# Kernel optimization log

Measured on AMD Instinct MI355X. Metric: run time of the kernel, lower is better.

Reference implementation:

```python
import jax, jax.numpy as jnp
import numpy as np

B, L, D = 8, 8192, 512
TARGET_RATIO = 1.0 / 6.0


def _normalize(v):
    # matches torch F.normalize(dim=-1, eps=1e-12)
    n = jnp.maximum(jnp.linalg.norm(v, axis=-1, keepdims=True), 1e-12)
    return v / n


def _downsample(x, b_hard):
    # vectorized stream compaction, padded to L (static upper bound of L_max)
    Bb, Ll, Dd = x.shape
    cnt = jnp.cumsum(b_hard.astype(jnp.int32), axis=1)
    pos = jnp.where(b_hard > 0.5, cnt - 1, Ll)          # non-selected -> dump slot L
    bidx = jnp.arange(Bb)[:, None]
    out = jnp.zeros((Bb, Ll + 1, Dd), x.dtype).at[bidx, pos].set(x)[:, :Ll]
    counts = cnt[:, -1]
    mask = jnp.arange(Ll)[None, :] < counts[:, None]
    return out, mask


def setup_inputs() -> dict:
    key = jax.random.key(0)
    k1, k2, k3 = jax.random.split(key, 3)
    x = jax.random.normal(k1, (B, L, D), jnp.float32)
    W_q = jax.random.normal(k2, (D, D), jnp.float32) / np.sqrt(D)
    W_k = jax.random.normal(k3, (D, D), jnp.float32) / np.sqrt(D)
    return {"x": x, "W_q": W_q, "W_k": W_k}


def reference(x, W_q, W_k):
    q = _normalize(jnp.einsum('bld,ed->ble', x, W_q))   # nn.Linear: x @ W.T
    k = _normalize(jnp.einsum('bld,ed->ble', x, W_k))
    k_prev = jnp.pad(k[:, :-1, :], ((0, 0), (1, 0), (0, 0)))
    cos_sim = jnp.sum(q * k_prev, axis=-1)               # (B, L)
    p = jnp.clip(0.5 * (1.0 - cos_sim), 0.0, 1.0)
    p = p.at[:, 0].set(1.0)                              # first position always boundary
    b_hard = (p >= 0.5).astype(x.dtype)
    N = 1.0 / TARGET_RATIO
    F_actual = jnp.mean(b_hard)
    G_actual = jnp.mean(p)
    ratio_loss = N / (N - 1.0) * ((N - 1.0) * F_actual * G_actual + (1.0 - F_actual) * (1.0 - G_actual))
    compressed, comp_mask = _downsample(x, b_hard)
    p_compressed, _ = _downsample(p[..., None], b_hard)
    p_compressed = p_compressed[..., 0]
    return (compressed, comp_mask, b_hard, p, p_compressed, ratio_loss)
```

## Files before the change

### kernel.cpp

```cpp
#include <hip/hip_runtime.h>
#include <hip/hip_bf16.h>
#include <math.h>

#define BB 8
#define LL 8192
#define DD 512
#define NROWS (BB * LL)

#define OUT_COMP   0
#define OUT_MASK   33554432
#define OUT_BHARD  33619968
#define OUT_P      33685504
#define OUT_PCOMP  33751040
#define OUT_LOSS   33816576

#define WS_FIXLIST 0
#define WS_FIXCNT  262144
#define WS_COUNTS  262148
#define WS_SUMP    262180
#define WS_SEL     262212
#define WS_SSK     524416
#define WS_SSQ     786560
#define WS_DOT     1048704
#define WS_WQH     1310848
#define WS_WKH     1835136

#define FIX_CAP 65536
#define FIX_TAU 4e-4f

typedef __attribute__((ext_vector_type(8))) _Float16 half8;
typedef __attribute__((ext_vector_type(4))) float f32x4;

static __device__ __forceinline__ void ld_g2l16(const void* g, void* l) {
  __builtin_amdgcn_global_load_lds(
      (const __attribute__((address_space(1))) void*)g,
      (__attribute__((address_space(3))) void*)l, 16, 0, 0);
}

__global__ __launch_bounds__(256) void wsplit(
    const float* __restrict__ Wq, const float* __restrict__ Wk,
    _Float16* __restrict__ wqh, _Float16* __restrict__ wkh,
    float* __restrict__ ssk, float* __restrict__ ssq,
    float* __restrict__ dotb, int* __restrict__ fixcnt) {
  const int t = blockIdx.x * 256 + threadIdx.x;
  if (t == 0) *fixcnt = 0;
  ssk[t] = 0.0f;
  ssq[t] = 0.0f;
  dotb[t] = 0.0f;

  const int m = t >> 15;
  const int c = t & 32767;
  const int kt = c >> 11;
  const int ct = (c >> 6) & 31;
  const int l = c & 63;
  const int n = l & 15;
  const int kblk = l >> 4;
  const int e = ct * 16 + n;
  const int d0 = kt * 32 + kblk * 8;
  const float* src = (m ? Wk : Wq) + (long)e * 512 + d0;
  _Float16* dh = (m ? wkh : wqh) + (long)c * 8;
  float4 v0 = *(const float4*)src;
  float4 v1 = *(const float4*)(src + 4);
  float av[8] = {v0.x, v0.y, v0.z, v0.w, v1.x, v1.y, v1.z, v1.w};
  half8 hi;
#pragma unroll
  for (int j = 0; j < 8; ++j) hi[j] = (_Float16)av[j];
  *(half8*)dh = hi;
}

__global__ __launch_bounds__(256, 2) void gemm_fused(
    const float* __restrict__ x,
    const _Float16* __restrict__ wqh, const _Float16* __restrict__ wkh,
    float* __restrict__ ssqOut, float* __restrict__ sskOut,
    float* __restrict__ dotOut,
    float* __restrict__ qedge, float* __restrict__ kedge) {
  __shared__ _Float16 smem[32768];
  _Float16* AH0 = smem;
  _Float16* AL0 = smem + 4096;
  _Float16* BQ0 = smem + 8192;
  _Float16* BK0 = smem + 12288;
  _Float16* AH1 = smem + 16384;
  _Float16* AL1 = smem + 20480;
  _Float16* BQ1 = smem + 24576;
  _Float16* BK1 = smem + 28672;

  const int tid = threadIdx.x;
  const int lane = tid & 63;
  const int w = tid >> 6;
  const int wrow = w & 1, wcol = w >> 1;
  const int g = lane >> 4, n = lane & 15;
  const int bx0 = blockIdx.x;
  const int bx = ((bx0 & 7) << 8) | (bx0 >> 3);
  const int rb = bx >> 2, cb = bx & 3;
  const long r0 = (long)rb * 128;

  const int arow = ((tid >> 6) << 4) | (tid & 15);
  const int akb = (tid >> 4) & 3;
  const float* ap = x + (r0 + arow) * 512 + akb * 8;

  f32x4 accq[4][4], acck[4][4];
#pragma unroll
  for (int mb = 0; mb < 4; ++mb)
#pragma unroll
    for (int nb = 0; nb < 4; ++nb) {
      accq[mb][nb] = (f32x4){0.f, 0.f, 0.f, 0.f};
      acck[mb][nb] = (f32x4){0.f, 0.f, 0.f, 0.f};
    }

#define STAGE_B(ktv, BQ_, BK_)                                            \
  do {                                                                    \
    const long bb = ((long)((ktv)*32 + cb * 8) << 9) + w * 1024 + lane * 8; \
    ld_g2l16(wqh + bb, (BQ_) + w * 1024);                                 \
    ld_g2l16(wqh + bb + 512, (BQ_) + w * 1024 + 512);                     \
    ld_g2l16(wkh + bb, (BK_) + w * 1024);                                 \
    ld_g2l16(wkh + bb + 512, (BK_) + w * 1024 + 512);                     \
  } while (0)

#define CONV_A(F0, F1, F2, F3, AH_, AL_)                                  \
  do {                                                                    \
    float av0[8] = {F0.x, F0.y, F0.z, F0.w, F1.x, F1.y, F1.z, F1.w};      \
    float av1[8] = {F2.x, F2.y, F2.z, F2.w, F3.x, F3.y, F3.z, F3.w};      \
    half8 h0, h1, l0, l1;                                                 \
    _Pragma("unroll") for (int j = 0; j < 8; ++j) {                       \
      _Float16 a = (_Float16)av0[j];                                      \
      h0[j] = a;                                                          \
      l0[j] = (_Float16)(av0[j] - (float)a);                              \
      _Float16 b = (_Float16)av1[j];                                      \
      h1[j] = b;                                                          \
      l1[j] = (_Float16)(av1[j] - (float)b);                              \
    }                                                                     \
    *(half8*)((AH_) + tid * 8) = h0;                                      \
    *(half8*)((AH_) + (tid + 256) * 8) = h1;                              \
    *(half8*)((AL_) + tid * 8) = l0;                                      \
    *(half8*)((AL_) + (tid + 256) * 8) = l1;                              \
  } while (0)

#define COMPUTE(AH_, AL_, BQ_, BK_)                                       \
  do {                                                                    \
    half8 ah[4], al[4], bq[4], bk[4];                                     \
    _Pragma("unroll") for (int mb = 0; mb < 4; ++mb) {                    \
      const int cm = wrow * 4 + mb;                                       \
      ah[mb] = *(const half8*)((AH_) + (cm * 64 + lane) * 8);             \
      al[mb] = *(const half8*)((AL_) + (cm * 64 + lane) * 8);             \
    }                                                                     \
    _Pragma("unroll") for (int nb = 0; nb < 4; ++nb) {                    \
      bq[nb] = *(const half8*)((BQ_) + ((wcol * 4 + nb) * 64 + lane) * 8);\
      bk[nb] = *(const half8*)((BK_) + ((wcol * 4 + nb) * 64 + lane) * 8);\
    }                                                                     \
    __builtin_amdgcn_s_setprio(1);                                        \
    _Pragma("unroll") for (int nb = 0; nb < 4; ++nb)                      \
        _Pragma("unroll") for (int mb = 0; mb < 4; ++mb) {                \
      accq[mb][nb] = __builtin_amdgcn_mfma_f32_16x16x32_f16(              \
          ah[mb], bq[nb], accq[mb][nb], 0, 0, 0);                         \
      acck[mb][nb] = __builtin_amdgcn_mfma_f32_16x16x32_f16(              \
          ah[mb], bk[nb], acck[mb][nb], 0, 0, 0);                         \
      accq[mb][nb] = __builtin_amdgcn_mfma_f32_16x16x32_f16(              \
          al[mb], bq[nb], accq[mb][nb], 0, 0, 0);                         \
      acck[mb][nb] = __builtin_amdgcn_mfma_f32_16x16x32_f16(              \
          al[mb], bk[nb], acck[mb][nb], 0, 0, 0);                         \
    }                                                                     \
    __builtin_amdgcn_s_setprio(0);                                        \
  } while (0)

  STAGE_B(0, BQ0, BK0);
  float4 pa0 = *(const float4*)(ap);
  float4 pa1 = *(const float4*)(ap + 4);
  float4 pa2 = *(const float4*)(ap + 64 * 512);
  float4 pa3 = *(const float4*)(ap + 64 * 512 + 4);
  CONV_A(pa0, pa1, pa2, pa3, AH0, AL0);
  float4 pb0 = *(const float4*)(ap + 32);
  float4 pb1 = *(const float4*)(ap + 32 + 4);
  float4 pb2 = *(const float4*)(ap + 32 + 64 * 512);
  float4 pb3 = *(const float4*)(ap + 32 + 64 * 512 + 4);
  __syncthreads();

  for (int i = 0; i < 8; ++i) {
    const int kt = 2 * i;
    STAGE_B(kt + 1, BQ1, BK1);
    CONV_A(pb0, pb1, pb2, pb3, AH1, AL1);
    if (i < 7) {
      const float* xp = ap + (kt + 2) * 32;
      pa0 = *(const float4*)(xp);
      pa1 = *(const float4*)(xp + 4);
      pa2 = *(const float4*)(xp + 64 * 512);
      pa3 = *(const float4*)(xp + 64 * 512 + 4);
    }
    COMPUTE(AH0, AL0, BQ0, BK0);
    __syncthreads();
    if (i < 7) {
      STAGE_B(kt + 2, BQ0, BK0);
      CONV_A(pa0, pa1, pa2, pa3, AH0, AL0);
      const float* xp2 = ap + (kt + 3) * 32;
      pb0 = *(const float4*)(xp2);
      pb1 = *(const float4*)(xp2 + 4);
      pb2 = *(const float4*)(xp2 + 64 * 512);
      pb3 = *(const float4*)(xp2 + 64 * 512 + 4);
    }
    COMPUTE(AH1, AL1, BQ1, BK1);
    __syncthreads();
  }

  _Float16* KX = smem;
  const int col0 = wcol * 64 + n;
  const int rbase = wrow * 64;
#pragma unroll
  for (int mb = 0; mb < 4; ++mb)
#pragma unroll
    for (int reg = 0; reg < 4; ++reg) {
      const int rl = rbase + mb * 16 + g * 4 + reg;
#pragma unroll
      for (int nb = 0; nb < 4; ++nb)
        KX[rl * 136 + col0 + nb * 16] = (_Float16)acck[mb][nb][reg];
    }
  __syncthreads();

  if (wrow == 1 && g == 3) {
#pragma unroll
    for (int nb = 0; nb < 4; ++nb)
      kedge[rb * 512 + cb * 128 + col0 + nb * 16] = acck[3][nb][3];
  }
  if (wrow == 0 && g == 0) {
#pragma unroll
    for (int nb = 0; nb < 4; ++nb)
      qedge[rb * 512 + cb * 128 + col0 + nb * 16] = accq[0][nb][0];
  }

#pragma unroll
  for (int mb = 0; mb < 4; ++mb) {
#pragma unroll
    for (int reg = 0; reg < 4; ++reg) {
      const int rl = rbase + mb * 16 + g * 4 + reg;
      const long row = r0 + rl;
      float sq = 0.f, sk = 0.f, dt = 0.f;
#pragma unroll
      for (int nb = 0; nb < 4; ++nb) {
        float qv = accq[mb][nb][reg];
        float kv = acck[mb][nb][reg];
        sq = fmaf(qv, qv, sq);
        sk = fmaf(kv, kv, sk);
        if (rl > 0) {
          float kp = (float)KX[(rl - 1) * 136 + col0 + nb * 16];
          dt = fmaf(qv, kp, dt);
        }
      }
#pragma unroll
      for (int m = 1; m < 16; m <<= 1) {
        sq += __shfl_xor(sq, m, 64);
        sk += __shfl_xor(sk, m, 64);
        dt += __shfl_xor(dt, m, 64);
      }
      if (n == 0) {
        atomicAdd(&ssqOut[row], sq);
        atomicAdd(&sskOut[row], sk);
        if (rl > 0) atomicAdd(&dotOut[row], dt);
      }
    }
  }
#undef STAGE_B
#undef CONV_A
#undef COMPUTE
}

__global__ __launch_bounds__(64) void edgedot(
    const float* __restrict__ qedge, const float* __restrict__ kedge,
    float* __restrict__ dotOut) {
  const int rb = blockIdx.x;
  if (rb == 0) return;
  const long row = (long)rb * 128;
  if ((row & (LL - 1)) == 0) return;
  const int lane = threadIdx.x;
  float dt = 0.f;
#pragma unroll
  for (int c = lane; c < 512; c += 64)
    dt = fmaf(qedge[rb * 512 + c], kedge[(rb - 1) * 512 + c], dt);
#pragma unroll
  for (int m = 1; m < 64; m <<= 1) dt += __shfl_xor(dt, m, 64);
  if (lane == 0) dotOut[row] = dt;
}

__global__ __launch_bounds__(256) void combine(
    const float* __restrict__ ssq, const float* __restrict__ ssk,
    const float* __restrict__ dotb, float* __restrict__ dout,
    int* __restrict__ fixlist, int* __restrict__ fixcnt) {
  const int r = blockIdx.x * 256 + threadIdx.x;
  const int l = r & (LL - 1);
  float p;
  float cosv = 0.0f;
  if (l != 0) {
    float nq = fmaxf(sqrtf(ssq[r]), 1e-12f);
    float nk = fmaxf(sqrtf(ssk[r - 1]), 1e-12f);
    cosv = dotb[r] / (nq * nk);
    p = fminf(fmaxf(0.5f * (1.0f - cosv), 0.0f), 1.0f);
  } else {
    p = 1.0f;
  }
  dout[OUT_P + r] = p;
  dout[OUT_BHARD + r] = (p >= 0.5f) ? 1.0f : 0.0f;
  if (l != 0 && fabsf(cosv) < FIX_TAU) {
    int idx = atomicAdd(fixcnt, 1);
    if (idx < FIX_CAP) fixlist[idx] = r;
  }
}

__global__ __launch_bounds__(256) void fixup(
    const float* __restrict__ x, const float* __restrict__ Wq,
    const float* __restrict__ Wk, float* __restrict__ dout,
    const int* __restrict__ fixlist, const int* __restrict__ fixcnt) {
  __shared__ float xr[512], xp[512];
  __shared__ double red[3][256];
  const int t = threadIdx.x;
  int nfix = *fixcnt;
  if (nfix > FIX_CAP) nfix = FIX_CAP;

  for (int idx = blockIdx.x; idx < nfix; idx += gridDim.x) {
    const int r = fixlist[idx];
    for (int d = t; d < 512; d += 256) {
      xr[d] = x[(long)r * 512 + d];
      xp[d] = x[(long)(r - 1) * 512 + d];
    }
    __syncthreads();
    double ssq = 0.0, ssk = 0.0, dot = 0.0;
    for (int e = t; e < 512; e += 256) {
      const float* wq = Wq + (long)e * 512;
      const float* wk = Wk + (long)e * 512;
      double q = 0.0, k = 0.0;
      for (int d = 0; d < 512; ++d) {
        q = fma((double)xr[d], (double)wq[d], q);
        k = fma((double)xp[d], (double)wk[d], k);
      }
      ssq += q * q;
      ssk += k * k;
      dot += q * k;
    }
    red[0][t] = ssq;
    red[1][t] = ssk;
    red[2][t] = dot;
    __syncthreads();
    for (int s = 128; s > 0; s >>= 1) {
      if (t < s) {
        red[0][t] += red[0][t + s];
        red[1][t] += red[1][t + s];
        red[2][t] += red[2][t + s];
      }
      __syncthreads();
    }
    if (t == 0) {
      double nq = sqrt(red[0][0]);
      double nk = sqrt(red[1][0]);
      if (nq < 1e-12) nq = 1e-12;
      if (nk < 1e-12) nk = 1e-12;
      float c = (float)(red[2][0] / (nq * nk));
      float p = fminf(fmaxf(0.5f * (1.0f - c), 0.0f), 1.0f);
      dout[OUT_P + r] = p;
      dout[OUT_BHARD + r] = (p >= 0.5f) ? 1.0f : 0.0f;
    }
    __syncthreads();
  }
}

__global__ __launch_bounds__(256) void scanb(
    float* __restrict__ dout, int* __restrict__ sel,
    int* __restrict__ counts, float* __restrict__ sump) {
  __shared__ int wtot[4];
  __shared__ float wps[4];
  const int b = blockIdx.x;
  const int t = threadIdx.x;
  const int lane = t & 63, wv = t >> 6;
  const long base = (long)b * LL;

  int cnt = 0;
  float psum = 0.0f;
#pragma unroll 4
  for (int j = 0; j < 32; ++j) {
    int l = t * 32 + j;
    float bh = dout[OUT_BHARD + base + l];
    float pv = dout[OUT_P + base + l];
    cnt += (bh > 0.5f) ? 1 : 0;
    psum += pv;
  }
  int inc = cnt;
#pragma unroll
  for (int off = 1; off < 64; off <<= 1) {
    int u = __shfl_up(inc, off, 64);
    if (lane >= off) inc += u;
  }
  float ps = psum;
#pragma unroll
  for (int off = 1; off < 64; off <<= 1) ps += __shfl_xor(ps, off, 64);
  if (lane == 63) wtot[wv] = inc;
  if (lane == 0) wps[wv] = ps;
  __syncthreads();
  int wbase = 0, total = 0;
#pragma unroll
  for (int i = 0; i < 4; ++i) {
    int c = wtot[i];
    if (i < wv) wbase += c;
    total += c;
  }
  if (t == 0) {
    counts[b] = total;
    sump[b] = wps[0] + wps[1] + wps[2] + wps[3];
  }
  for (int j = 0; j < 32; ++j) {
    int l = t * 32 + j;
    dout[OUT_MASK + base + l] = (l < total) ? 1.0f : 0.0f;
    dout[OUT_PCOMP + base + l] = 0.0f;
  }
  __syncthreads();
  int pos = wbase + inc - cnt;
  for (int j = 0; j < 32; ++j) {
    int l = t * 32 + j;
    float bh = dout[OUT_BHARD + base + l];
    if (bh > 0.5f) {
      dout[OUT_PCOMP + base + pos] = dout[OUT_P + base + l];
      sel[base + pos] = l;
      ++pos;
    }
  }
}

__global__ void lossk(float* __restrict__ dout, const int* __restrict__ counts,
                      const float* __restrict__ sump) {
  if (threadIdx.x == 0 && blockIdx.x == 0) {
    float fc = 0.0f, gs = 0.0f;
    for (int b = 0; b < BB; ++b) {
      fc += (float)counts[b];
      gs += sump[b];
    }
    float F = fc / (float)NROWS;
    float G = gs / (float)NROWS;
    dout[OUT_LOSS] = 1.2f * (5.0f * F * G + (1.0f - F) * (1.0f - G));
  }
}

__global__ __launch_bounds__(128) void emit(
    const float* __restrict__ x, float* __restrict__ dout,
    const int* __restrict__ sel, const int* __restrict__ counts) {
  const long bid = blockIdx.x;
  const int b = (int)(bid >> 13);
  const int j = (int)(bid & (LL - 1));
  const int cnt = counts[b];
  float4 v = make_float4(0.0f, 0.0f, 0.0f, 0.0f);
  if (j < cnt) {
    const int l = sel[((long)b << 13) + j];
    v = *(const float4*)(x + (((long)b << 13) + l) * 512 + threadIdx.x * 4);
  }
  *(float4*)(dout + OUT_COMP + (((long)b << 13) + j) * 512 + threadIdx.x * 4) = v;
}

extern "C" void kernel_launch(void* const* d_in, const int* in_sizes, int n_in,
                              void* d_out, int out_size, void* d_ws,
                              size_t ws_size, hipStream_t stream) {
  const float* x = (const float*)d_in[0];
  const float* Wq = (const float*)d_in[1];
  const float* Wk = (const float*)d_in[2];
  float* out = (float*)d_out;
  char* ws = (char*)d_ws;

  int* fixlist = (int*)(ws + WS_FIXLIST);
  int* fixcnt = (int*)(ws + WS_FIXCNT);
  int* counts = (int*)(ws + WS_COUNTS);
  float* sump = (float*)(ws + WS_SUMP);
  int* sel = (int*)(ws + WS_SEL);
  float* ssk = (float*)(ws + WS_SSK);
  float* ssq = (float*)(ws + WS_SSQ);
  float* dotb = (float*)(ws + WS_DOT);
  _Float16* wqh = (_Float16*)(ws + WS_WQH);
  _Float16* wkh = (_Float16*)(ws + WS_WKH);

  float* kedge = (float*)(out + OUT_COMP);
  float* qedge = (float*)(out + OUT_COMP + 262144);

  wsplit<<<256, 256, 0, stream>>>(Wq, Wk, wqh, wkh, ssk, ssq, dotb, fixcnt);
  gemm_fused<<<2048, 256, 0, stream>>>(x, wqh, wkh, ssq, ssk, dotb, qedge, kedge);
  edgedot<<<512, 64, 0, stream>>>(qedge, kedge, dotb);
  combine<<<NROWS / 256, 256, 0, stream>>>(ssq, ssk, dotb, out, fixlist, fixcnt);
  fixup<<<512, 256, 0, stream>>>(x, Wq, Wk, out, fixlist, fixcnt);
  scanb<<<BB, 256, 0, stream>>>(out, sel, counts, sump);
  lossk<<<1, 64, 0, stream>>>(out, counts, sump);
  emit<<<NROWS, 128, 0, stream>>>(x, out, sel, counts);
}
```

Baseline: 533.3 us.

## Load weight fragments directly from global into registers, shrink LDS

The fused GEMM no longer stages the fp16 Wq/Wk tiles through LDS with global_load_lds. Each wave now reads its B fragments straight from global (L2-resident) memory into registers, and LDS holds only the A hi/lo buffers. This cuts shared memory use, which may allow more occupancy, and removes LDS traffic. Barriers now wait only on lgkmcnt, and the fix-up tolerance is tightened to 1e-4. The risk is global-load latency on the MFMA critical path, plus more rows going to the fix-up path.

```diff
diff --git a/kernel.cpp b/kernel.cpp
--- a/kernel.cpp
+++ b/kernel.cpp
@@ -26,16 +26,17 @@
 #define WS_WKH     1835136
 
 #define FIX_CAP 65536
-#define FIX_TAU 4e-4f
+#define FIX_TAU 1e-4f
 
 typedef __attribute__((ext_vector_type(8))) _Float16 half8;
 typedef __attribute__((ext_vector_type(4))) float f32x4;
 
-static __device__ __forceinline__ void ld_g2l16(const void* g, void* l) {
-  __builtin_amdgcn_global_load_lds(
-      (const __attribute__((address_space(1))) void*)g,
-      (__attribute__((address_space(3))) void*)l, 16, 0, 0);
-}
+#define BARRIER()                                          \
+  do {                                                     \
+    asm volatile("s_waitcnt lgkmcnt(0)" ::: "memory");     \
+    __builtin_amdgcn_sched_barrier(0);                     \
+    __builtin_amdgcn_s_barrier();                          \
+  } while (0)
 
 __global__ __launch_bounds__(256) void wsplit(
     const float* __restrict__ Wq, const float* __restrict__ Wk,
@@ -74,15 +75,11 @@
     float* __restrict__ ssqOut, float* __restrict__ sskOut,
     float* __restrict__ dotOut,
     float* __restrict__ qedge, float* __restrict__ kedge) {
-  __shared__ _Float16 smem[32768];
+  __shared__ _Float16 smem[17408];
   _Float16* AH0 = smem;
   _Float16* AL0 = smem + 4096;
-  _Float16* BQ0 = smem + 8192;
-  _Float16* BK0 = smem + 12288;
-  _Float16* AH1 = smem + 16384;
-  _Float16* AL1 = smem + 20480;
-  _Float16* BQ1 = smem + 24576;
-  _Float16* BK1 = smem + 28672;
+  _Float16* AH1 = smem + 8192;
+  _Float16* AL1 = smem + 12288;
 
   const int tid = threadIdx.x;
   const int lane = tid & 63;
@@ -98,6 +95,9 @@
   const int akb = (tid >> 4) & 3;
   const float* ap = x + (r0 + arow) * 512 + akb * 8;
 
+  const _Float16* bqb = wqh + ((long)((cb * 8 + wcol * 4) * 64 + lane)) * 8;
+  const _Float16* bkb = wkh + ((long)((cb * 8 + wcol * 4) * 64 + lane)) * 8;
+
   f32x4 accq[4][4], acck[4][4];
 #pragma unroll
   for (int mb = 0; mb < 4; ++mb)
@@ -106,15 +106,6 @@
       accq[mb][nb] = (f32x4){0.f, 0.f, 0.f, 0.f};
       acck[mb][nb] = (f32x4){0.f, 0.f, 0.f, 0.f};
     }
-
-#define STAGE_B(ktv, BQ_, BK_)                                            \
-  do {                                                                    \
-    const long bb = ((long)((ktv)*32 + cb * 8) << 9) + w * 1024 + lane * 8; \
-    ld_g2l16(wqh + bb, (BQ_) + w * 1024);                                 \
-    ld_g2l16(wqh + bb + 512, (BQ_) + w * 1024 + 512);                     \
-    ld_g2l16(wkh + bb, (BK_) + w * 1024);                                 \
-    ld_g2l16(wkh + bb + 512, (BK_) + w * 1024 + 512);                     \
-  } while (0)
 
 #define CONV_A(F0, F1, F2, F3, AH_, AL_)                                  \
   do {                                                                    \
@@ -135,17 +126,19 @@
     *(half8*)((AL_) + (tid + 256) * 8) = l1;                              \
   } while (0)
 
-#define COMPUTE(AH_, AL_, BQ_, BK_)                                       \
+#define COMPUTE(AH_, AL_, KTV)                                            \
   do {                                                                    \
-    half8 ah[4], al[4], bq[4], bk[4];                                     \
+    const _Float16* bqp = bqb + (long)(KTV) * 16384;                      \
+    const _Float16* bkp = bkb + (long)(KTV) * 16384;                      \
+    half8 bq[4], bk[4], ah[4], al[4];                                     \
+    _Pragma("unroll") for (int nb = 0; nb < 4; ++nb) {                    \
+      bq[nb] = *(const half8*)(bqp + nb * 512);                           \
+      bk[nb] = *(const half8*)(bkp + nb * 512);                           \
+    }                                                                     \
     _Pragma("unroll") for (int mb = 0; mb < 4; ++mb) {                    \
       const int cm = wrow * 4 + mb;                                       \
       ah[mb] = *(const half8*)((AH_) + (cm * 64 + lane) * 8);             \
       al[mb] = *(const half8*)((AL_) + (cm * 64 + lane) * 8);             \
-    }                                                                     \
-    _Pragma("unroll") for (int nb = 0; nb < 4; ++nb) {                    \
-      bq[nb] = *(const half8*)((BQ_) + ((wcol * 4 + nb) * 64 + lane) * 8);\
-      bk[nb] = *(const half8*)((BK_) + ((wcol * 4 + nb) * 64 + lane) * 8);\
     }                                                                     \
     __builtin_amdgcn_s_setprio(1);                                        \
     _Pragma("unroll") for (int nb = 0; nb < 4; ++nb)                      \
@@ -162,7 +155,6 @@
     __builtin_amdgcn_s_setprio(0);                                        \
   } while (0)
 
-  STAGE_B(0, BQ0, BK0);
   float4 pa0 = *(const float4*)(ap);
   float4 pa1 = *(const float4*)(ap + 4);
   float4 pa2 = *(const float4*)(ap + 64 * 512);
@@ -172,11 +164,10 @@
   float4 pb1 = *(const float4*)(ap + 32 + 4);
   float4 pb2 = *(const float4*)(ap + 32 + 64 * 512);
   float4 pb3 = *(const float4*)(ap + 32 + 64 * 512 + 4);
-  __syncthreads();
+  BARRIER();
 
   for (int i = 0; i < 8; ++i) {
     const int kt = 2 * i;
-    STAGE_B(kt + 1, BQ1, BK1);
     CONV_A(pb0, pb1, pb2, pb3, AH1, AL1);
     if (i < 7) {
       const float* xp = ap + (kt + 2) * 32;
@@ -185,10 +176,9 @@
       pa2 = *(const float4*)(xp + 64 * 512);
       pa3 = *(const float4*)(xp + 64 * 512 + 4);
     }
-    COMPUTE(AH0, AL0, BQ0, BK0);
-    __syncthreads();
+    COMPUTE(AH0, AL0, kt);
+    BARRIER();
     if (i < 7) {
-      STAGE_B(kt + 2, BQ0, BK0);
       CONV_A(pa0, pa1, pa2, pa3, AH0, AL0);
       const float* xp2 = ap + (kt + 3) * 32;
       pb0 = *(const float4*)(xp2);
@@ -196,8 +186,8 @@
       pb2 = *(const float4*)(xp2 + 64 * 512);
       pb3 = *(const float4*)(xp2 + 64 * 512 + 4);
     }
-    COMPUTE(AH1, AL1, BQ1, BK1);
-    __syncthreads();
+    COMPUTE(AH1, AL1, kt + 1);
+    BARRIER();
   }
 
   _Float16* KX = smem;
@@ -256,7 +246,6 @@
       }
     }
   }
-#undef STAGE_B
 #undef CONV_A
 #undef COMPUTE
 }
```

Result: faster. 487.2 us (-8.6%).

## Hand-schedule GEMM pipeline with explicit waitcnt barriers and reordered prefetch

Applied to the files above, without the earlier changes.

Replaces __syncthreads in the fused fp16-split GEMM main loop with explicit `s_waitcnt vmcnt(4)`/`lgkmcnt(0)` plus `s_barrier`, fenced by `sched_barrier`. This lets the next tile's global x loads stay in flight across the barrier. Global loads are issued before the fp32-to-fp16 conversion, and tail prefetches are made unconditional with clamped indices so the loop body is uniform. The LDS buffer layout and the LDS read order (B before A) are rearranged. The fixup threshold FIX_TAU is lowered, which changes how many rows take the exact recompute path. Clamped tail loads add some redundant memory traffic, and the hand-set wait counts rely on the exact instruction order.

```diff
diff --git a/kernel.cpp b/kernel.cpp
--- a/kernel.cpp
+++ b/kernel.cpp
@@ -26,7 +26,7 @@
 #define WS_WKH     1835136
 
 #define FIX_CAP 65536
-#define FIX_TAU 4e-4f
+#define FIX_TAU 1e-4f
 
 typedef __attribute__((ext_vector_type(8))) _Float16 half8;
 typedef __attribute__((ext_vector_type(4))) float f32x4;
@@ -77,10 +77,10 @@
   __shared__ _Float16 smem[32768];
   _Float16* AH0 = smem;
   _Float16* AL0 = smem + 4096;
-  _Float16* BQ0 = smem + 8192;
-  _Float16* BK0 = smem + 12288;
-  _Float16* AH1 = smem + 16384;
-  _Float16* AL1 = smem + 20480;
+  _Float16* AH1 = smem + 8192;
+  _Float16* AL1 = smem + 12288;
+  _Float16* BQ0 = smem + 16384;
+  _Float16* BK0 = smem + 20480;
   _Float16* BQ1 = smem + 24576;
   _Float16* BK1 = smem + 28672;
 
@@ -107,13 +107,13 @@
       acck[mb][nb] = (f32x4){0.f, 0.f, 0.f, 0.f};
     }
 
-#define STAGE_B(ktv, BQ_, BK_)                                            \
-  do {                                                                    \
+#define STAGE_B(ktv, BQ_, BK_)                                              \
+  do {                                                                      \
     const long bb = ((long)((ktv)*32 + cb * 8) << 9) + w * 1024 + lane * 8; \
-    ld_g2l16(wqh + bb, (BQ_) + w * 1024);                                 \
-    ld_g2l16(wqh + bb + 512, (BQ_) + w * 1024 + 512);                     \
-    ld_g2l16(wkh + bb, (BK_) + w * 1024);                                 \
-    ld_g2l16(wkh + bb + 512, (BK_) + w * 1024 + 512);                     \
+    ld_g2l16(wqh + bb, (BQ_) + w * 1024);                                   \
+    ld_g2l16(wqh + bb + 512, (BQ_) + w * 1024 + 512);                       \
+    ld_g2l16(wkh + bb, (BK_) + w * 1024);                                   \
+    ld_g2l16(wkh + bb + 512, (BK_) + w * 1024 + 512);                       \
   } while (0)
 
 #define CONV_A(F0, F1, F2, F3, AH_, AL_)                                  \
@@ -138,14 +138,14 @@
 #define COMPUTE(AH_, AL_, BQ_, BK_)                                       \
   do {                                                                    \
     half8 ah[4], al[4], bq[4], bk[4];                                     \
+    _Pragma("unroll") for (int nb = 0; nb < 4; ++nb) {                    \
+      bq[nb] = *(const half8*)((BQ_) + ((wcol * 4 + nb) * 64 + lane) * 8);\
+      bk[nb] = *(const half8*)((BK_) + ((wcol * 4 + nb) * 64 + lane) * 8);\
+    }                                                                     \
     _Pragma("unroll") for (int mb = 0; mb < 4; ++mb) {                    \
       const int cm = wrow * 4 + mb;                                       \
       ah[mb] = *(const half8*)((AH_) + (cm * 64 + lane) * 8);             \
       al[mb] = *(const half8*)((AL_) + (cm * 64 + lane) * 8);             \
-    }                                                                     \
-    _Pragma("unroll") for (int nb = 0; nb < 4; ++nb) {                    \
-      bq[nb] = *(const half8*)((BQ_) + ((wcol * 4 + nb) * 64 + lane) * 8);\
-      bk[nb] = *(const half8*)((BK_) + ((wcol * 4 + nb) * 64 + lane) * 8);\
     }                                                                     \
     __builtin_amdgcn_s_setprio(1);                                        \
     _Pragma("unroll") for (int nb = 0; nb < 4; ++nb)                      \
@@ -157,48 +157,74 @@
       accq[mb][nb] = __builtin_amdgcn_mfma_f32_16x16x32_f16(              \
           al[mb], bq[nb], accq[mb][nb], 0, 0, 0);                         \
       acck[mb][nb] = __builtin_amdgcn_mfma_f32_16x16x32_f16(              \
-          al[mb], bk[nb], acck[mb][nb], 0, 0, 0);                         \
+          al[mb], bk[nb], acck[mb][nb], 0, 0, 0);                        \
     }                                                                     \
     __builtin_amdgcn_s_setprio(0);                                        \
   } while (0)
 
+#define BARRIER_CNT()                                       \
+  do {                                                      \
+    asm volatile("s_waitcnt vmcnt(4)" ::: "memory");        \
+    asm volatile("s_waitcnt lgkmcnt(0)" ::: "memory");      \
+    __builtin_amdgcn_sched_barrier(0);                      \
+    __builtin_amdgcn_s_barrier();                           \
+  } while (0)
+
+#define FENCE() __builtin_amdgcn_sched_barrier(0)
+
   STAGE_B(0, BQ0, BK0);
+  FENCE();
   float4 pa0 = *(const float4*)(ap);
   float4 pa1 = *(const float4*)(ap + 4);
   float4 pa2 = *(const float4*)(ap + 64 * 512);
   float4 pa3 = *(const float4*)(ap + 64 * 512 + 4);
+  FENCE();
   CONV_A(pa0, pa1, pa2, pa3, AH0, AL0);
   float4 pb0 = *(const float4*)(ap + 32);
   float4 pb1 = *(const float4*)(ap + 32 + 4);
   float4 pb2 = *(const float4*)(ap + 32 + 64 * 512);
   float4 pb3 = *(const float4*)(ap + 32 + 64 * 512 + 4);
-  __syncthreads();
+  FENCE();
+  BARRIER_CNT();
 
   for (int i = 0; i < 8; ++i) {
     const int kt = 2 * i;
     STAGE_B(kt + 1, BQ1, BK1);
-    CONV_A(pb0, pb1, pb2, pb3, AH1, AL1);
-    if (i < 7) {
-      const float* xp = ap + (kt + 2) * 32;
+    FENCE();
+    {
+      const int ktn = (kt + 2 < 16) ? (kt + 2) : 15;
+      const float* xp = ap + ktn * 32;
       pa0 = *(const float4*)(xp);
       pa1 = *(const float4*)(xp + 4);
       pa2 = *(const float4*)(xp + 64 * 512);
       pa3 = *(const float4*)(xp + 64 * 512 + 4);
     }
+    FENCE();
+    CONV_A(pb0, pb1, pb2, pb3, AH1, AL1);
     COMPUTE(AH0, AL0, BQ0, BK0);
-    __syncthreads();
-    if (i < 7) {
-      STAGE_B(kt + 2, BQ0, BK0);
-      CONV_A(pa0, pa1, pa2, pa3, AH0, AL0);
-      const float* xp2 = ap + (kt + 3) * 32;
+    BARRIER_CNT();
+    {
+      const int ktn = (kt + 2 < 16) ? (kt + 2) : 15;
+      STAGE_B(ktn, BQ0, BK0);
+    }
+    FENCE();
+    {
+      const int ktn = (kt + 3 < 16) ? (kt + 3) : 15;
+      const float* xp2 = ap + ktn * 32;
       pb0 = *(const float4*)(xp2);
       pb1 = *(const float4*)(xp2 + 4);
       pb2 = *(const float4*)(xp2 + 64 * 512);
       pb3 = *(const float4*)(xp2 + 64 * 512 + 4);
     }
+    FENCE();
+    CONV_A(pa0, pa1, pa2, pa3, AH0, AL0);
     COMPUTE(AH1, AL1, BQ1, BK1);
-    __syncthreads();
-  }
+    BARRIER_CNT();
+  }
+
+  asm volatile("s_waitcnt vmcnt(0)" ::: "memory");
+  __builtin_amdgcn_sched_barrier(0);
+  __syncthreads();
 
   _Float16* KX = smem;
   const int col0 = wcol * 64 + n;
@@ -259,6 +285,8 @@
 #undef STAGE_B
 #undef CONV_A
 #undef COMPUTE
+#undef BARRIER_CNT
+#undef FENCE
 }
 
 __global__ __launch_bounds__(64) void edgedot(
```

New measurement: 468.7 us. 1.14x faster.
